# Performance work log

Measured on AMD Instinct MI355X. Metric: run time of the kernel, lower is better.

## Reference

```python
import jax, jax.numpy as jnp
import numpy as np

N_NODES = 100000
N_EDGES = 1600000
D = 64
L = 3


def setup_inputs() -> dict:
    key = jax.random.key(0)
    ks = jax.random.split(key, 6)
    x = jax.random.normal(ks[0], (N_NODES, D), dtype=jnp.float32)
    edges = jax.random.randint(ks[1], (2, N_EDGES), 0, N_NODES, dtype=jnp.int64)
    scale = 1.0 / np.sqrt(D)
    W_phi = jax.random.normal(ks[2], (L, D, D), dtype=jnp.float32) * scale
    W_theta = jax.random.normal(ks[3], (L, D, D), dtype=jnp.float32) * scale
    W_out = jax.random.normal(ks[4], (1, D), dtype=jnp.float32) * scale
    b_out = jax.random.normal(ks[5], (1,), dtype=jnp.float32) * scale
    return {"x": x, "edges": edges, "W_phi": W_phi, "W_theta": W_theta,
            "W_out": W_out, "b_out": b_out}


def _devconv(x, Wp, Wt, src, dst):
    # DevConv: out_i = W_theta @ max_{j in N(i)} W_phi (x_j - x_i)
    diff = x[src] - x[dst]                 # [E, D] irregular gather
    msg = diff @ Wp.T                      # [E, D]
    agg = jax.ops.segment_max(msg, dst, num_segments=N_NODES)  # [N, D]
    agg = jnp.where(jnp.isneginf(agg), 0.0, agg)  # isolated nodes -> 0
    return agg @ Wt.T


def reference(x, edges, W_phi, W_theta, W_out, b_out):
    src, dst = edges[0], edges[1]
    for l in range(L):
        x = _devconv(x, W_phi[l], W_theta[l], src, dst)
    scores = (x @ W_out.T + b_out)[:, 0]   # Linear(D,1) then squeeze(-1)
    return jax.nn.sigmoid(scores)
```

## Files before the change

kernel.cpp:

```cpp
#include <hip/hip_runtime.h>
#include <math.h>


#define WBITS 8
#define WNODES 256
#define MAXNB 512
#define CHUNK 4096
#define STG_CAP 12288

#define PKNINF 0xFC00FC00u

typedef __fp16 h2v __attribute__((ext_vector_type(2)));
typedef _Float16 f16x8 __attribute__((ext_vector_type(8)));
typedef float f32x4 __attribute__((ext_vector_type(4)));

__device__ __forceinline__ unsigned pkmax(unsigned a, unsigned b) {
    unsigned r;
    asm("v_pk_max_f16 %0, %1, %2" : "=v"(r) : "v"(a), "v"(b));
    return r;
}
__device__ __forceinline__ unsigned pkrtz(float a, float b) {
    h2v r = __builtin_amdgcn_cvt_pkrtz(a, b);
    return *reinterpret_cast<unsigned*>(&r);
}
__device__ __forceinline__ float h2lo(unsigned u) {
    h2v h = *reinterpret_cast<h2v*>(&u);
    return (float)h.x;
}
__device__ __forceinline__ float h2hi(unsigned u) {
    h2v h = *reinterpret_cast<h2v*>(&u);
    return (float)h.y;
}

#define G8(K0) do { \
    int j0 = __builtin_amdgcn_ds_swizzle(myc, (((K0)+0)<<5)|0x10); \
    int j1 = __builtin_amdgcn_ds_swizzle(myc, (((K0)+1)<<5)|0x10); \
    int j2 = __builtin_amdgcn_ds_swizzle(myc, (((K0)+2)<<5)|0x10); \
    int j3 = __builtin_amdgcn_ds_swizzle(myc, (((K0)+3)<<5)|0x10); \
    int j4 = __builtin_amdgcn_ds_swizzle(myc, (((K0)+4)<<5)|0x10); \
    int j5 = __builtin_amdgcn_ds_swizzle(myc, (((K0)+5)<<5)|0x10); \
    int j6 = __builtin_amdgcn_ds_swizzle(myc, (((K0)+6)<<5)|0x10); \
    int j7 = __builtin_amdgcn_ds_swizzle(myc, (((K0)+7)<<5)|0x10); \
    uint2 w0 = y16[(size_t)j0 * 16 + t]; \
    uint2 w1 = y16[(size_t)j1 * 16 + t]; \
    uint2 w2 = y16[(size_t)j2 * 16 + t]; \
    uint2 w3 = y16[(size_t)j3 * 16 + t]; \
    uint2 w4 = y16[(size_t)j4 * 16 + t]; \
    uint2 w5 = y16[(size_t)j5 * 16 + t]; \
    uint2 w6 = y16[(size_t)j6 * 16 + t]; \
    uint2 w7 = y16[(size_t)j7 * 16 + t]; \
    c0 = pkmax(c0, pkmax(pkmax(pkmax(w0.x, w1.x), pkmax(w2.x, w3.x)), \
                         pkmax(pkmax(w4.x, w5.x), pkmax(w6.x, w7.x)))); \
    c1 = pkmax(c1, pkmax(pkmax(pkmax(w0.y, w1.y), pkmax(w2.y, w3.y)), \
                         pkmax(pkmax(w4.y, w5.y), pkmax(w6.y, w7.y)))); \
} while (0)

__global__ __launch_bounds__(256) void prep_k(
    const float* __restrict__ Wp, const float* __restrict__ Wt,
    const float* __restrict__ Wout,
    __fp16* __restrict__ Wh, float* __restrict__ vout,
    int* __restrict__ bcnt, int* __restrict__ gcur,
    int* __restrict__ row_ptr, int N, int E)
{
    __shared__ float A[4096];
    __shared__ float B[4096];
    int tid = threadIdx.x;
    int b = blockIdx.x;
    if (b < 2) {
        if (b == 0) {
            for (int i = tid; i < MAXNB; i += 256) { bcnt[i] = 0; gcur[i] = 0; }
        } else if (tid == 0) {
            row_ptr[N] = E;
        }
        const float* Ap = Wp + (size_t)(b + 1) * 4096;
        const float* Bp = Wt + (size_t)b * 4096;
        for (int i = tid; i < 4096; i += 256) { A[i] = Ap[i]; B[i] = Bp[i]; }
        __syncthreads();
        __fp16* C = Wh + (size_t)(b + 1) * 4096;
        for (int i = tid; i < 4096; i += 256) {
            int d = i >> 6, k = i & 63;
            float s = 0.f;
            #pragma unroll
            for (int m = 0; m < 64; ++m) s += A[d * 64 + m] * B[m * 64 + k];
            C[i] = (__fp16)s;
        }
    } else {
        for (int i = tid; i < 4096; i += 256) {
            A[i] = Wt[2 * 4096 + i];
            Wh[i] = (__fp16)Wp[i];
        }
        if (tid < 64) B[tid] = Wout[tid];
        __syncthreads();
        if (tid < 64) {
            float s = 0.f;
            #pragma unroll
            for (int m = 0; m < 64; ++m) s += B[m] * A[m * 64 + tid];
            vout[tid] = s;
        }
    }
}

__global__ __launch_bounds__(256) void hist_gemm_k(
    const int* __restrict__ eidx, int* __restrict__ bcnt, int E, int NB,
    int chunkBlocks,
    const float* __restrict__ xin, const __fp16* __restrict__ W,
    unsigned short* __restrict__ y16o, int n)
{
    __shared__ int h[MAXNB];
    int tid = threadIdx.x;
    if (blockIdx.x < chunkBlocks) {
        for (int i = tid; i < MAXNB; i += 256) h[i] = 0;
        __syncthreads();
        int start = blockIdx.x * CHUNK;
        int end = min(E, start + CHUNK);
        for (int e = start + tid; e < end; e += 256)
            atomicAdd(&h[eidx[E + e] >> WBITS], 1);
        __syncthreads();
        for (int i = tid; i < NB; i += 256)
            if (h[i]) atomicAdd(&bcnt[i], h[i]);
    } else {
        int lane = tid & 63;
        int wid  = tid >> 6;
        int r0   = ((blockIdx.x - chunkBlocks) * 4 + wid) * 16;
        if (r0 >= n) return;
        int l15 = lane & 15;
        int ko  = (lane >> 4) * 8;

        f16x8 af[4][2];
        #pragma unroll
        for (int dt = 0; dt < 4; ++dt)
            #pragma unroll
            for (int kf = 0; kf < 2; ++kf)
                af[dt][kf] = *(const f16x8*)(W + (size_t)(dt * 16 + l15) * 64 + ko + kf * 32);

        f16x8 bf[2];
        int rr = min(r0 + l15, n - 1);
        #pragma unroll
        for (int kf = 0; kf < 2; ++kf) {
            const float4* p = (const float4*)(xin + (size_t)rr * 64 + ko + kf * 32);
            float4 a = p[0], b = p[1];
            union { uint4 u; f16x8 hh; } cv;
            cv.u.x = pkrtz(a.x, a.y); cv.u.y = pkrtz(a.z, a.w);
            cv.u.z = pkrtz(b.x, b.y); cv.u.w = pkrtz(b.z, b.w);
            bf[kf] = cv.hh;
        }

        int r = r0 + l15;
        int d4 = (lane >> 4) * 4;
        #pragma unroll
        for (int dt = 0; dt < 4; ++dt) {
            f32x4 acc = {0.f, 0.f, 0.f, 0.f};
            acc = __builtin_amdgcn_mfma_f32_16x16x32_f16(af[dt][0], bf[0], acc, 0, 0, 0);
            acc = __builtin_amdgcn_mfma_f32_16x16x32_f16(af[dt][1], bf[1], acc, 0, 0, 0);
            if (r < n) {
                uint2 p; p.x = pkrtz(acc[0], acc[1]); p.y = pkrtz(acc[2], acc[3]);
                *(uint2*)(y16o + (size_t)r * 64 + dt * 16 + d4) = p;
            }
        }
    }
}

__global__ __launch_bounds__(256) void partA_k(
    const int* __restrict__ eidx, const int* __restrict__ bcnt,
    int* __restrict__ gcur, int* __restrict__ B1, int E, int NB)
{
    __shared__ int hist[MAXNB];
    __shared__ int lofs[MAXNB];
    __shared__ int lcur[MAXNB];
    __shared__ int gofs[MAXNB];
    __shared__ int sA[MAXNB], sB[MAXNB];
    __shared__ int stg_val[CHUNK];
    __shared__ int stg_pos[CHUNK];
    int tid = threadIdx.x;
    int start = blockIdx.x * CHUNK;
    int cnt = min(E - start, CHUNK);
    if (cnt <= 0) return;

    for (int i = tid; i < MAXNB; i += 256) hist[i] = 0;
    __syncthreads();

    int es[CHUNK / 256], ed[CHUNK / 256];
    #pragma unroll
    for (int i = 0; i < CHUNK / 256; ++i) {
        int li = i * 256 + tid;
        if (li < cnt) {
            es[i] = eidx[start + li];
            ed[i] = eidx[E + start + li];
            atomicAdd(&hist[ed[i] >> WBITS], 1);
        }
    }
    __syncthreads();
    for (int i = tid; i < MAXNB; i += 256) sA[i] = (i < NB) ? bcnt[i] : 0;
    __syncthreads();
    int* sp = sA; int* dp = sB;
    for (int off = 1; off < MAXNB; off <<= 1) {
        for (int i = tid; i < MAXNB; i += 256)
            dp[i] = sp[i] + ((i >= off) ? sp[i - off] : 0);
        __syncthreads();
        int* t = sp; sp = dp; dp = t;
    }
    for (int i = tid; i < MAXNB; i += 256)
        gofs[i] = sp[i] - ((i < NB) ? bcnt[i] : 0);
    __syncthreads();
    for (int i = tid; i < MAXNB; i += 256) sp[i] = hist[i];
    __syncthreads();
    for (int off = 1; off < MAXNB; off <<= 1) {
        for (int i = tid; i < MAXNB; i += 256)
            dp[i] = sp[i] + ((i >= off) ? sp[i - off] : 0);
        __syncthreads();
        int* t = sp; sp = dp; dp = t;
    }
    for (int i = tid; i < MAXNB; i += 256) {
        int c  = hist[i];
        int ex = sp[i] - c;
        lofs[i] = ex;
        lcur[i] = ex;
        if (c) gofs[i] += atomicAdd(&gcur[i], c);
    }
    __syncthreads();
    #pragma unroll
    for (int i = 0; i < CHUNK / 256; ++i) {
        int li = i * 256 + tid;
        if (li < cnt) {
            int b = ed[i] >> WBITS;
            int p = atomicAdd(&lcur[b], 1);
            stg_val[p] = es[i] | ((ed[i] & (WNODES - 1)) << 17);
            stg_pos[p] = gofs[b] + (p - lofs[b]);
        }
    }
    __syncthreads();
    for (int i = tid; i < cnt; i += 256)
        B1[stg_pos[i]] = stg_val[i];
}

__global__ __launch_bounds__(256) void partB_k(
    const int* __restrict__ B1, const int* __restrict__ bcnt,
    int* __restrict__ row_ptr, int* __restrict__ col, int N, int NB)
{
    __shared__ int cnt[WNODES];
    __shared__ int lcur[WNODES];
    __shared__ int sA[MAXNB], sB[MAXNB];
    __shared__ int stg[STG_CAP];
    int b   = blockIdx.x;
    int tid = threadIdx.x;

    for (int i = tid; i < MAXNB; i += 256) sA[i] = (i < NB) ? bcnt[i] : 0;
    __syncthreads();
    int* sp = sA; int* dp = sB;
    for (int off = 1; off < MAXNB; off <<= 1) {
        for (int i = tid; i < MAXNB; i += 256)
            dp[i] = sp[i] + ((i >= off) ? sp[i - off] : 0);
        __syncthreads();
        int* t = sp; sp = dp; dp = t;
    }
    int gb1 = sp[b];
    int gb0 = gb1 - bcnt[b];
    int m   = gb1 - gb0;
    int nb0 = b << WBITS;

    if (tid < WNODES) cnt[tid] = 0;
    __syncthreads();
    for (int i = tid; i < m; i += 256)
        atomicAdd(&cnt[B1[gb0 + i] >> 17], 1);
    __syncthreads();
    int v0 = (tid < WNODES) ? cnt[tid] : 0;
    sA[tid] = v0;
    __syncthreads();
    sp = sA; dp = sB;
    for (int off = 1; off < WNODES; off <<= 1) {
        dp[tid] = sp[tid] + ((tid >= off) ? sp[tid - off] : 0);
        __syncthreads();
        int* t = sp; sp = dp; dp = t;
    }
    if (tid < WNODES) {
        int ex = sp[tid] - v0;
        lcur[tid] = ex;
        int node = nb0 + tid;
        if (node < N) row_ptr[node] = gb0 + ex;
    }
    __syncthreads();
    if (m <= STG_CAP) {
        for (int i = tid; i < m; i += 256) {
            int v = B1[gb0 + i];
            int p = atomicAdd(&lcur[v >> 17], 1);
            stg[p] = v & 0x1FFFF;
        }
        __syncthreads();
        for (int i = tid; i < m; i += 256)
            col[gb0 + i] = stg[i];
    } else {
        for (int i = tid; i < m; i += 256) {
            int v = B1[gb0 + i];
            int p = atomicAdd(&lcur[v >> 17], 1);
            col[gb0 + p] = v & 0x1FFFF;
        }
    }
}

template<bool HEAD>
__global__ __launch_bounds__(256) void gather_fused_k(
    const int* __restrict__ rp, const int* __restrict__ col,
    const uint2* __restrict__ y16,
    const __fp16* __restrict__ W,
    unsigned short* __restrict__ y16o,
    const float* __restrict__ vv, const float* __restrict__ bptr,
    float* __restrict__ out, int n)
{
    __shared__ __fp16 sAgg[4][16][80];
    int lane = threadIdx.x & 63;
    int wid  = threadIdx.x >> 6;
    int q = lane >> 4, t = lane & 15;
    int base = blockIdx.x * 64 + wid * 16;

    for (int p = 0; p < 4; ++p) {
        int node  = base + p * 4 + q;
        bool alive = node < n;
        int beg = 0, cnt = 0;
        if (alive) { beg = rp[node]; cnt = rp[node + 1] - beg; }
        unsigned c0 = PKNINF, c1 = PKNINF;
        if (cnt > 0) {
            int pcnt = (cnt + 7) & ~7;
            int e = 0;
            while (e < pcnt) {
                int myc = col[beg + min(e + t, cnt - 1)];
                G8(0);
                if (e + 8 < pcnt) { G8(8); }
                e += 16;
            }
        }
        if (alive) {
            bool has = cnt > 0;
            uint2 yi2 = y16[(size_t)node * 16 + t];
            float g0 = has ? (h2lo(c0) - h2lo(yi2.x)) : 0.f;
            float g1 = has ? (h2hi(c0) - h2hi(yi2.x)) : 0.f;
            float g2 = has ? (h2lo(c1) - h2lo(yi2.y)) : 0.f;
            float g3 = has ? (h2hi(c1) - h2hi(yi2.y)) : 0.f;
            if (!HEAD) {
                uint2 pk; pk.x = pkrtz(g0, g1); pk.y = pkrtz(g2, g3);
                *(uint2*)&sAgg[wid][p * 4 + q][4 * t] = pk;
            } else {
                float4 vp = ((const float4*)vv)[t];
                float s = g0 * vp.x + g1 * vp.y + g2 * vp.z + g3 * vp.w;
                s += __shfl_xor(s, 8);
                s += __shfl_xor(s, 4);
                s += __shfl_xor(s, 2);
                s += __shfl_xor(s, 1);
                if (t == 0)
                    out[node] = 1.f / (1.f + __expf(-(s + bptr[0])));
            }
        } else if (!HEAD) {
            uint2 z; z.x = 0u; z.y = 0u;
            *(uint2*)&sAgg[wid][p * 4 + q][4 * t] = z;
        }
    }

    if (!HEAD) {
        __syncthreads();
        f16x8 af[4][2];
        #pragma unroll
        for (int dt = 0; dt < 4; ++dt)
            #pragma unroll
            for (int kf = 0; kf < 2; ++kf)
                af[dt][kf] = *(const f16x8*)(W + (size_t)(dt * 16 + t) * 64 + q * 8 + kf * 32);
        f16x8 bf[2];
        #pragma unroll
        for (int kf = 0; kf < 2; ++kf)
            bf[kf] = *(const f16x8*)&sAgg[wid][t][q * 8 + kf * 32];

        int r = base + t;
        int d4 = q * 4;
        #pragma unroll
        for (int dt = 0; dt < 4; ++dt) {
            f32x4 acc = {0.f, 0.f, 0.f, 0.f};
            acc = __builtin_amdgcn_mfma_f32_16x16x32_f16(af[dt][0], bf[0], acc, 0, 0, 0);
            acc = __builtin_amdgcn_mfma_f32_16x16x32_f16(af[dt][1], bf[1], acc, 0, 0, 0);
            if (r < n) {
                uint2 pk; pk.x = pkrtz(acc[0], acc[1]); pk.y = pkrtz(acc[2], acc[3]);
                *(uint2*)(y16o + (size_t)r * 64 + dt * 16 + d4) = pk;
            }
        }
    }
}

extern "C" void kernel_launch(void* const* d_in, const int* in_sizes, int n_in,
                              void* d_out, int out_size, void* d_ws, size_t ws_size,
                              hipStream_t stream)
{
    const float* x     = (const float*)d_in[0];
    const int*   edges = (const int*)d_in[1];
    const float* Wp    = (const float*)d_in[2];
    const float* Wt    = (const float*)d_in[3];
    const float* Wout  = (const float*)d_in[4];
    const float* bout  = (const float*)d_in[5];
    const int N = in_sizes[0] / 64;
    const int E = in_sizes[1] / 2;
    const int NB = (N + WNODES - 1) >> WBITS;
    float* out = (float*)d_out;

    char* ws = (char*)d_ws;
    unsigned short* y16A = (unsigned short*)ws; ws += (size_t)N * 64 * 2;
    unsigned short* y16B = (unsigned short*)ws; ws += (size_t)N * 64 * 2;
    int*   B1  = (int*)y16B;
    int* col     = (int*)ws; ws += (size_t)(E + 8) * 4;
    int* row_ptr = (int*)ws; ws += (size_t)(N + 4) * 4;
    int* bcnt    = (int*)ws; ws += MAXNB * 4;
    int* gcur    = (int*)ws; ws += MAXNB * 4;
    __fp16* Wh = (__fp16*)ws; ws += 3 * 4096 * 2;
    float*  vv = (float*)ws;  ws += 64 * 4;

    const int chunkBlocks = (E + CHUNK - 1) / CHUNK;
    const int gemmBlocks  = ((N + 15) / 16 + 3) / 4;
    const int fusedBlocks = (N + 63) / 64;

    prep_k<<<3, 256, 0, stream>>>(Wp, Wt, Wout, Wh, vv, bcnt, gcur, row_ptr, N, E);

    hist_gemm_k<<<chunkBlocks + gemmBlocks, 256, 0, stream>>>(
        edges, bcnt, E, NB, chunkBlocks, x, Wh, y16A, N);
    partA_k<<<chunkBlocks, 256, 0, stream>>>(edges, bcnt, gcur, B1, E, NB);
    partB_k<<<NB, 256, 0, stream>>>(B1, bcnt, row_ptr, col, N, NB);

    gather_fused_k<false><<<fusedBlocks, 256, 0, stream>>>(
        row_ptr, col, (const uint2*)y16A, Wh + 4096, y16B,
        nullptr, nullptr, nullptr, N);
    gather_fused_k<false><<<fusedBlocks, 256, 0, stream>>>(
        row_ptr, col, (const uint2*)y16B, Wh + 8192, y16A,
        nullptr, nullptr, nullptr, N);
    gather_fused_k<true><<<fusedBlocks, 256, 0, stream>>>(
        row_ptr, col, (const uint2*)y16A, nullptr, nullptr,
        vv, bout, out, N);
}
```

Baseline: 183.8 us.

## Regroup preprocessing kernels: merge weight prep with histogram, GEMM with partition

Moves the per-chunk destination histogram into the weight-prep kernel and the first-layer MFMA GEMM into the partition (partA) kernel. This removes one kernel launch and lets the GEMM overlap with the scatter pass instead of the histogram. The bcnt/gcur zeroing now uses hipMemsetAsync, which relies on gcur sitting directly after bcnt in the workspace. partA_gemm_k carries the large shared-memory footprint of partA into the GEMM blocks, which may lower occupancy for them.

```diff
diff --git a/kernel.cpp b/kernel.cpp
--- a/kernel.cpp
+++ b/kernel.cpp
@@ -55,23 +55,32 @@
                          pkmax(pkmax(w4.y, w5.y), pkmax(w6.y, w7.y)))); \
 } while (0)
 
-__global__ __launch_bounds__(256) void prep_k(
+__global__ __launch_bounds__(256) void prep_hist_k(
     const float* __restrict__ Wp, const float* __restrict__ Wt,
     const float* __restrict__ Wout,
     __fp16* __restrict__ Wh, float* __restrict__ vout,
-    int* __restrict__ bcnt, int* __restrict__ gcur,
-    int* __restrict__ row_ptr, int N, int E)
+    int* __restrict__ row_ptr, int N, int E,
+    const int* __restrict__ eidx, int* __restrict__ bcnt, int NB)
 {
     __shared__ float A[4096];
     __shared__ float B[4096];
+    __shared__ int h[MAXNB];
     int tid = threadIdx.x;
     int b = blockIdx.x;
+    if (b >= 3) {
+        for (int i = tid; i < MAXNB; i += 256) h[i] = 0;
+        __syncthreads();
+        int start = (b - 3) * CHUNK;
+        int end = min(E, start + CHUNK);
+        for (int e = start + tid; e < end; e += 256)
+            atomicAdd(&h[eidx[E + e] >> WBITS], 1);
+        __syncthreads();
+        for (int i = tid; i < NB; i += 256)
+            if (h[i]) atomicAdd(&bcnt[i], h[i]);
+        return;
+    }
     if (b < 2) {
-        if (b == 0) {
-            for (int i = tid; i < MAXNB; i += 256) { bcnt[i] = 0; gcur[i] = 0; }
-        } else if (tid == 0) {
-            row_ptr[N] = E;
-        }
+        if (b == 1 && tid == 0) row_ptr[N] = E;
         const float* Ap = Wp + (size_t)(b + 1) * 4096;
         const float* Bp = Wt + (size_t)b * 4096;
         for (int i = tid; i < 4096; i += 256) { A[i] = Ap[i]; B[i] = Bp[i]; }
@@ -100,69 +109,12 @@
     }
 }
 
-__global__ __launch_bounds__(256) void hist_gemm_k(
-    const int* __restrict__ eidx, int* __restrict__ bcnt, int E, int NB,
+__global__ __launch_bounds__(256) void partA_gemm_k(
+    const int* __restrict__ eidx, const int* __restrict__ bcnt,
+    int* __restrict__ gcur, int* __restrict__ B1, int E, int NB,
     int chunkBlocks,
     const float* __restrict__ xin, const __fp16* __restrict__ W,
     unsigned short* __restrict__ y16o, int n)
-{
-    __shared__ int h[MAXNB];
-    int tid = threadIdx.x;
-    if (blockIdx.x < chunkBlocks) {
-        for (int i = tid; i < MAXNB; i += 256) h[i] = 0;
-        __syncthreads();
-        int start = blockIdx.x * CHUNK;
-        int end = min(E, start + CHUNK);
-        for (int e = start + tid; e < end; e += 256)
-            atomicAdd(&h[eidx[E + e] >> WBITS], 1);
-        __syncthreads();
-        for (int i = tid; i < NB; i += 256)
-            if (h[i]) atomicAdd(&bcnt[i], h[i]);
-    } else {
-        int lane = tid & 63;
-        int wid  = tid >> 6;
-        int r0   = ((blockIdx.x - chunkBlocks) * 4 + wid) * 16;
-        if (r0 >= n) return;
-        int l15 = lane & 15;
-        int ko  = (lane >> 4) * 8;
-
-        f16x8 af[4][2];
-        #pragma unroll
-        for (int dt = 0; dt < 4; ++dt)
-            #pragma unroll
-            for (int kf = 0; kf < 2; ++kf)
-                af[dt][kf] = *(const f16x8*)(W + (size_t)(dt * 16 + l15) * 64 + ko + kf * 32);
-
-        f16x8 bf[2];
-        int rr = min(r0 + l15, n - 1);
-        #pragma unroll
-        for (int kf = 0; kf < 2; ++kf) {
-            const float4* p = (const float4*)(xin + (size_t)rr * 64 + ko + kf * 32);
-            float4 a = p[0], b = p[1];
-            union { uint4 u; f16x8 hh; } cv;
-            cv.u.x = pkrtz(a.x, a.y); cv.u.y = pkrtz(a.z, a.w);
-            cv.u.z = pkrtz(b.x, b.y); cv.u.w = pkrtz(b.z, b.w);
-            bf[kf] = cv.hh;
-        }
-
-        int r = r0 + l15;
-        int d4 = (lane >> 4) * 4;
-        #pragma unroll
-        for (int dt = 0; dt < 4; ++dt) {
-            f32x4 acc = {0.f, 0.f, 0.f, 0.f};
-            acc = __builtin_amdgcn_mfma_f32_16x16x32_f16(af[dt][0], bf[0], acc, 0, 0, 0);
-            acc = __builtin_amdgcn_mfma_f32_16x16x32_f16(af[dt][1], bf[1], acc, 0, 0, 0);
-            if (r < n) {
-                uint2 p; p.x = pkrtz(acc[0], acc[1]); p.y = pkrtz(acc[2], acc[3]);
-                *(uint2*)(y16o + (size_t)r * 64 + dt * 16 + d4) = p;
-            }
-        }
-    }
-}
-
-__global__ __launch_bounds__(256) void partA_k(
-    const int* __restrict__ eidx, const int* __restrict__ bcnt,
-    int* __restrict__ gcur, int* __restrict__ B1, int E, int NB)
 {
     __shared__ int hist[MAXNB];
     __shared__ int lofs[MAXNB];
@@ -172,6 +124,48 @@
     __shared__ int stg_val[CHUNK];
     __shared__ int stg_pos[CHUNK];
     int tid = threadIdx.x;
+    if (blockIdx.x >= chunkBlocks) {
+        int lane = tid & 63;
+        int wid  = tid >> 6;
+        int r0   = ((blockIdx.x - chunkBlocks) * 4 + wid) * 16;
+        if (r0 >= n) return;
+        int l15 = lane & 15;
+        int ko  = (lane >> 4) * 8;
+
+        f16x8 af[4][2];
+        #pragma unroll
+        for (int dt = 0; dt < 4; ++dt)
+            #pragma unroll
+            for (int kf = 0; kf < 2; ++kf)
+                af[dt][kf] = *(const f16x8*)(W + (size_t)(dt * 16 + l15) * 64 + ko + kf * 32);
+
+        f16x8 bf[2];
+        int rr = min(r0 + l15, n - 1);
+        #pragma unroll
+        for (int kf = 0; kf < 2; ++kf) {
+            const float4* p = (const float4*)(xin + (size_t)rr * 64 + ko + kf * 32);
+            float4 a = p[0], b = p[1];
+            union { uint4 u; f16x8 hh; } cv;
+            cv.u.x = pkrtz(a.x, a.y); cv.u.y = pkrtz(a.z, a.w);
+            cv.u.z = pkrtz(b.x, b.y); cv.u.w = pkrtz(b.z, b.w);
+            bf[kf] = cv.hh;
+        }
+
+        int r = r0 + l15;
+        int d4 = (lane >> 4) * 4;
+        #pragma unroll
+        for (int dt = 0; dt < 4; ++dt) {
+            f32x4 acc = {0.f, 0.f, 0.f, 0.f};
+            acc = __builtin_amdgcn_mfma_f32_16x16x32_f16(af[dt][0], bf[0], acc, 0, 0, 0);
+            acc = __builtin_amdgcn_mfma_f32_16x16x32_f16(af[dt][1], bf[1], acc, 0, 0, 0);
+            if (r < n) {
+                uint2 p; p.x = pkrtz(acc[0], acc[1]); p.y = pkrtz(acc[2], acc[3]);
+                *(uint2*)(y16o + (size_t)r * 64 + dt * 16 + d4) = p;
+            }
+        }
+        return;
+    }
+
     int start = blockIdx.x * CHUNK;
     int cnt = min(E - start, CHUNK);
     if (cnt <= 0) return;
@@ -412,11 +406,14 @@
     const int gemmBlocks  = ((N + 15) / 16 + 3) / 4;
     const int fusedBlocks = (N + 63) / 64;
 
-    prep_k<<<3, 256, 0, stream>>>(Wp, Wt, Wout, Wh, vv, bcnt, gcur, row_ptr, N, E);
-
-    hist_gemm_k<<<chunkBlocks + gemmBlocks, 256, 0, stream>>>(
-        edges, bcnt, E, NB, chunkBlocks, x, Wh, y16A, N);
-    partA_k<<<chunkBlocks, 256, 0, stream>>>(edges, bcnt, gcur, B1, E, NB);
+    hipMemsetAsync(bcnt, 0, 2 * MAXNB * sizeof(int), stream);
+
+    prep_hist_k<<<3 + chunkBlocks, 256, 0, stream>>>(
+        Wp, Wt, Wout, Wh, vv, row_ptr, N, E, edges, bcnt, NB);
+
+    partA_gemm_k<<<chunkBlocks + gemmBlocks, 256, 0, stream>>>(
+        edges, bcnt, gcur, B1, E, NB, chunkBlocks, x, Wh, y16A, N);
+
     partB_k<<<NB, 256, 0, stream>>>(B1, bcnt, row_ptr, col, N, NB);
 
     gather_fused_k<false><<<fusedBlocks, 256, 0, stream>>>(
```

Result: faster. 179.3 us (-2.4%).
